# Performance work log

Hardware: AMD Instinct MI355X
Metric: run time of the kernel (lower is better)

The kernel has to match this reference:

```python
import jax, jax.numpy as jnp
import numpy as np
from jax import lax

B, CIN, COUT, FES, H, W, K = 32, 64, 64, 3, 128, 128, 3
DN = ('NCHW', 'OIHW', 'NCHW')
PAD = [(1, 1), (1, 1)]


def setup_inputs() -> dict:
    key = jax.random.key(0)
    ks = jax.random.split(key, 6)
    fan_main = CIN * K * K
    fan_extra = FES * K * K
    return {
        'x': jax.random.normal(ks[0], (B, CIN, H, W), jnp.float32),
        'extra_inputs': jax.random.normal(ks[1], (B, COUT * FES), jnp.float32),
        'conv_w': jax.random.normal(ks[2], (COUT, CIN, K, K), jnp.float32) / np.sqrt(fan_main),
        'conv_b': jax.random.normal(ks[3], (COUT,), jnp.float32) * 0.01,
        # extra_w[i] is the weight of extra_convs[i] (shape [1, FES, K, K]) stacked over i
        'extra_w': jax.random.normal(ks[4], (COUT, FES, K, K), jnp.float32) / np.sqrt(fan_extra),
        'extra_b': jax.random.normal(ks[5], (COUT,), jnp.float32) * 0.01,
    }


def reference(x, extra_inputs, conv_w, conv_b, extra_w, extra_b):
    # main conv: [B, CIN, H, W] -> [B, COUT, H, W]
    main_out = lax.conv_general_dilated(x, conv_w, (1, 1), PAD, dimension_numbers=DN)
    main_out = main_out + conv_b[None, :, None, None]

    b, _, h, w = x.shape
    cout = extra_w.shape[0]
    # spatially-constant broadcast of the per-sample embedding vector:
    # [B, COUT*FES] -> [B, COUT*FES, H, W]
    ein = jnp.broadcast_to(extra_inputs[:, :, None, None], (b, extra_inputs.shape[1], h, w))
    # the per-channel python loop of tiny convs == one grouped conv with
    # feature_group_count = COUT (each group: FES in-channels -> 1 out-channel)
    extra_out = lax.conv_general_dilated(ein, extra_w, (1, 1), PAD,
                                         dimension_numbers=DN,
                                         feature_group_count=cout)
    extra_out = extra_out + extra_b[None, :, None, None]
    return main_out + extra_out
```

## Files before the change

### kernel.cpp

```cpp
#include <hip/hip_runtime.h>

#define HH 128
#define WW 128
#define SB0 73728
#define SBN 26112

typedef __bf16 bf16x8 __attribute__((ext_vector_type(8)));
typedef __bf16 bf16x2 __attribute__((ext_vector_type(2)));
typedef float f32x4 __attribute__((ext_vector_type(4)));

static __device__ __forceinline__ unsigned short f2bf(float f) {
  unsigned int u = __float_as_uint(f);
  u = (u + 0x7FFFu + ((u >> 16) & 1u)) >> 16;
  return (unsigned short)u;
}

static __device__ __forceinline__ unsigned int pack2bf(float lo, float hi) {
  bf16x2 v;
  v[0] = (__bf16)lo;
  v[1] = (__bf16)hi;
  return __builtin_bit_cast(unsigned int, v);
}

__global__ __launch_bounds__(256) void prep_wfrag(const float* __restrict__ conv_w,
                                                  unsigned short* __restrict__ wfrag) {
  int tid = blockIdx.x * 256 + threadIdx.x;
  if (tid >= 18 * 2048) return;
  int i    = tid & 7;
  int lane = (tid >> 3) & 63;
  int cot  = (tid >> 9) & 3;
  int f    = tid >> 11;
  int h    = f / 9;
  int tap  = f - h * 9;
  int co   = cot * 16 + (lane & 15);
  int ci   = h * 32 + (lane >> 4) * 8 + i;
  wfrag[tid] = f2bf(conv_w[(co * 64 + ci) * 9 + tap]);
}

__global__ __launch_bounds__(256) void prep_ext(const float* __restrict__ extra_in,
                                                const float* __restrict__ extra_w,
                                                const float* __restrict__ conv_b,
                                                const float* __restrict__ extra_b,
                                                float* __restrict__ ext) {
  int t = blockIdx.x * 256 + threadIdx.x;
  if (t >= 32 * 64) return;
  int b = t >> 6, co = t & 63;
  float base = conv_b[co] + extra_b[co];
  float acc[3][3];
#pragma unroll
  for (int i = 0; i < 3; ++i)
#pragma unroll
    for (int j = 0; j < 3; ++j) acc[i][j] = 0.f;

#pragma unroll
  for (int f = 0; f < 3; ++f) {
    float e = extra_in[b * 192 + co * 3 + f];
    const float* w = extra_w + (co * 3 + f) * 9;
    float rs[3][3];
#pragma unroll
    for (int ky = 0; ky < 3; ++ky) {
      float w0 = w[ky * 3 + 0], w1 = w[ky * 3 + 1], w2 = w[ky * 3 + 2];
      rs[ky][0] = w1 + w2;
      rs[ky][1] = w0 + w1 + w2;
      rs[ky][2] = w0 + w1;
    }
#pragma unroll
    for (int cx = 0; cx < 3; ++cx) {
      acc[0][cx] += e * (rs[1][cx] + rs[2][cx]);
      acc[1][cx] += e * (rs[0][cx] + rs[1][cx] + rs[2][cx]);
      acc[2][cx] += e * (rs[0][cx] + rs[1][cx]);
    }
  }
#pragma unroll
  for (int cy = 0; cy < 3; ++cy)
#pragma unroll
    for (int cx = 0; cx < 3; ++cx)
      ext[t * 9 + cy * 3 + cx] = base + acc[cy][cx];
}

__global__ __launch_bounds__(512, 1) void conv_pc(const float* __restrict__ x,
                                                  const unsigned short* __restrict__ wfrag,
                                                  const float* __restrict__ ext,
                                                  float* __restrict__ out) {
  const int orig = blockIdx.x + 2 * (blockIdx.y + 4 * blockIdx.z);
  const int work = (orig & 7) * 32 + (orig >> 3);
  const int xh    = work & 1;
  const int yq    = (work >> 1) & 3;
  const int b     = work >> 3;

  const int ybase = yq * 32;
  const int x0    = xh * 64;
  const int tid  = threadIdx.x;
  const int lane = tid & 63;
  const int wv8  = tid >> 6;
  const int grp  = wv8 >> 2;
  const int wv   = wv8 & 3;
  const int gtid = tid & 255;
  const int pix  = lane & 15;
  const int g    = lane >> 4;

  __shared__ __align__(16) unsigned char lds[SB0 + 3 * SBN];

  const float* xb   = x + (size_t)b * 64 * HH * WW;
  const float* extb = ext + (size_t)b * 64 * 9;

#pragma unroll
  for (int it = 0; it < 9; ++it) {
    int off = (tid + it * 512) * 16;
    __builtin_amdgcn_global_load_lds(
        (const __attribute__((address_space(1))) unsigned int*)((const char*)wfrag + off),
        (__attribute__((address_space(3))) unsigned int*)(lds + off), 16, 0, 0);
  }

  auto stage_to = [&](int buf, int c, int h) {
    unsigned char* sb = lds + SB0 + buf * SBN;
#pragma unroll
    for (int it = 0; it < 2; ++it) {
      int q = gtid + it * 256;
      if (q < 384) {
        int qd  = q & 15;
        int cig = (q >> 4) & 3;
        int r   = q >> 6;
        int gy  = ybase + 4 * c - 1 + r;
        int cc  = 1 + 4 * qd;
        int x_in = x0 + 4 * qd;
        float4 f[8];
        if ((unsigned)gy < 128u) {
          const float* src = xb + (size_t)(h * 32 + cig * 8) * (HH * WW) + gy * WW + x_in;
#pragma unroll
          for (int j = 0; j < 8; ++j) f[j] = *(const float4*)(src + (size_t)j * (HH * WW));
        } else {
#pragma unroll
          for (int j = 0; j < 8; ++j) f[j] = make_float4(0.f, 0.f, 0.f, 0.f);
        }
#pragma unroll
        for (int p = 0; p < 4; ++p) {
          const int cp = cc + p;
          unsigned int pk[4];
#pragma unroll
          for (int w = 0; w < 4; ++w) {
            const float* lo = (const float*)&f[2 * w];
            const float* hi = (const float*)&f[2 * w + 1];
            pk[w] = pack2bf(lo[p], hi[p]);
          }
          int byte = ((r * 68 + cp) * 64 + cig * 16) ^ (((cp ^ (cp >> 2)) & 3) << 4);
          *(uint4*)(sb + byte) = make_uint4(pk[0], pk[1], pk[2], pk[3]);
        }
      }
    }
    if (gtid < 48) {
      int cc  = (gtid & 1) ? 65 : 0;
      int cig = (gtid >> 1) & 3;
      int r   = gtid >> 3;
      int gy  = ybase + 4 * c - 1 + r;
      int x_in = x0 - 1 + cc;
      bool inb = ((unsigned)gy < 128u) & ((unsigned)x_in < 128u);
      unsigned int pk[4] = {0u, 0u, 0u, 0u};
      if (inb) {
        const float* src = xb + (size_t)(h * 32 + cig * 8) * (HH * WW) + gy * WW + x_in;
        float v[8];
#pragma unroll
        for (int j = 0; j < 8; ++j) v[j] = src[(size_t)j * (HH * WW)];
#pragma unroll
        for (int w = 0; w < 4; ++w) pk[w] = pack2bf(v[2 * w], v[2 * w + 1]);
      }
      int byte = ((r * 68 + cc) * 64 + cig * 16) ^ (((cc ^ (cc >> 2)) & 3) << 4);
      *(uint4*)(sb + byte) = make_uint4(pk[0], pk[1], pk[2], pk[3]);
    }
  };

  if (grp == 0) stage_to(0, 0, 0);
  else          stage_to(1, 0, 1);
  __syncthreads();

  f32x4 acc[4][4];

#pragma unroll 1
  for (int p = 0; p < 16; ++p) {
    const int c = p >> 1, h = p & 1, buf = p % 3;
    if ((c & 1) == grp) {
      if (h == 0) {
#pragma unroll
        for (int i = 0; i < 4; ++i)
#pragma unroll
          for (int j = 0; j < 4; ++j) acc[i][j] = (f32x4){0.f, 0.f, 0.f, 0.f};
      }
      const unsigned char* sb = lds + SB0 + buf * SBN;
#pragma unroll
      for (int tap = 0; tap < 9; ++tap) {
        const int ky = tap / 3, kx = tap - ky * 3;
        bf16x8 af[4];
#pragma unroll
        for (int cot = 0; cot < 4; ++cot)
          af[cot] = *(const bf16x8*)(lds + (h * 9 + tap) * 4096 + cot * 1024 + lane * 16);
        bf16x8 pf[4];
        const int r = wv + ky;
#pragma unroll
        for (int m = 0; m < 4; ++m) {
          int cc = m * 16 + pix + kx;
          int byte = ((r * 68 + cc) * 64 + g * 16) ^ (((cc ^ (cc >> 2)) & 3) << 4);
          pf[m] = *(const bf16x8*)(sb + byte);
        }
#pragma unroll
        for (int cot = 0; cot < 4; ++cot)
#pragma unroll
          for (int m = 0; m < 4; ++m)
            acc[cot][m] = __builtin_amdgcn_mfma_f32_16x16x32_bf16(af[cot], pf[m],
                                                                  acc[cot][m], 0, 0, 0);
      }
      if (h == 1) {
        const int y  = ybase + 4 * c + wv;
        const int cy = (y == 0) ? 0 : ((y == HH - 1) ? 2 : 1);
#pragma unroll
        for (int cot = 0; cot < 4; ++cot) {
#pragma unroll
          for (int m = 0; m < 4; ++m) {
            int xg = x0 + m * 16 + pix;
            int cx = (xg == 0) ? 0 : ((xg == WW - 1) ? 2 : 1);
#pragma unroll
            for (int j = 0; j < 4; ++j) {
              int co = cot * 16 + g * 4 + j;
              out[(((size_t)b * 64 + co) * HH + y) * WW + xg] =
                  acc[cot][m][j] + extb[co * 9 + cy * 3 + cx];
            }
          }
        }
      }
    } else {
      const int p2 = p + 2;
      if (p2 < 16) stage_to(p2 % 3, p2 >> 1, p2 & 1);
    }
    __syncthreads();
  }
}

extern "C" void kernel_launch(void* const* d_in, const int* in_sizes, int n_in,
                              void* d_out, int out_size, void* d_ws, size_t ws_size,
                              hipStream_t stream) {
  const float* x        = (const float*)d_in[0];
  const float* extra_in = (const float*)d_in[1];
  const float* conv_w   = (const float*)d_in[2];
  const float* conv_b   = (const float*)d_in[3];
  const float* extra_w  = (const float*)d_in[4];
  const float* extra_b  = (const float*)d_in[5];
  float* out = (float*)d_out;

  unsigned short* wfrag = (unsigned short*)d_ws;
  float* ext = (float*)((char*)d_ws + 73728);

  hipLaunchKernelGGL(prep_wfrag, dim3(144), dim3(256), 0, stream, conv_w, wfrag);
  hipLaunchKernelGGL(prep_ext,   dim3(8),   dim3(256), 0, stream,
                     extra_in, extra_w, conv_b, extra_b, ext);
  hipLaunchKernelGGL(conv_pc, dim3(2, 4, 32), dim3(512), 0, stream,
                     x, wfrag, ext, out);
}
```

Baseline: 72.95 us.

## Split conv into many small blocks over output-channel halves and merge prep kernels

Replaces the persistent-style 256-block conv kernel (512 threads, triple-buffered LDS pipeline over 8 row chunks) with 4096 small 256-thread blocks. Each block handles 4 rows, 64 columns and one half of the output channels, with two blocks per CU. The aim is more blocks in flight and occupancy-based latency hiding in place of the explicit producer/consumer pipeline. In exchange, each input tile is loaded and bf16-converted twice (once per channel half), halo rows are re-read across row tiles, and weight fragments are reloaded per block. The two prep kernels are also fused into one launch.

Result: slower. 90.87 us (+24.6%).

```diff
diff --git a/kernel.cpp b/kernel.cpp
--- a/kernel.cpp
+++ b/kernel.cpp
@@ -2,8 +2,7 @@
 
 #define HH 128
 #define WW 128
-#define SB0 73728
-#define SBN 26112
+#define SBUF 36864
 
 typedef __bf16 bf16x8 __attribute__((ext_vector_type(8)));
 typedef __bf16 bf16x2 __attribute__((ext_vector_type(2)));
@@ -22,27 +21,28 @@
   return __builtin_bit_cast(unsigned int, v);
 }
 
-__global__ __launch_bounds__(256) void prep_wfrag(const float* __restrict__ conv_w,
-                                                  unsigned short* __restrict__ wfrag) {
-  int tid = blockIdx.x * 256 + threadIdx.x;
-  if (tid >= 18 * 2048) return;
-  int i    = tid & 7;
-  int lane = (tid >> 3) & 63;
-  int cot  = (tid >> 9) & 3;
-  int f    = tid >> 11;
-  int h    = f / 9;
-  int tap  = f - h * 9;
-  int co   = cot * 16 + (lane & 15);
-  int ci   = h * 32 + (lane >> 4) * 8 + i;
-  wfrag[tid] = f2bf(conv_w[(co * 64 + ci) * 9 + tap]);
-}
-
-__global__ __launch_bounds__(256) void prep_ext(const float* __restrict__ extra_in,
+__global__ __launch_bounds__(256) void prep_all(const float* __restrict__ conv_w,
+                                                const float* __restrict__ extra_in,
                                                 const float* __restrict__ extra_w,
                                                 const float* __restrict__ conv_b,
                                                 const float* __restrict__ extra_b,
+                                                unsigned short* __restrict__ wfrag,
                                                 float* __restrict__ ext) {
-  int t = blockIdx.x * 256 + threadIdx.x;
+  if (blockIdx.x < 144) {
+    int tid = blockIdx.x * 256 + threadIdx.x;
+    if (tid >= 18 * 2048) return;
+    int i    = tid & 7;
+    int lane = (tid >> 3) & 63;
+    int cot  = (tid >> 9) & 3;
+    int f    = tid >> 11;
+    int h    = f / 9;
+    int tap  = f - h * 9;
+    int co   = cot * 16 + (lane & 15);
+    int ci   = h * 32 + (lane >> 4) * 8 + i;
+    wfrag[tid] = f2bf(conv_w[(co * 64 + ci) * 9 + tap]);
+    return;
+  }
+  int t = (blockIdx.x - 144) * 256 + threadIdx.x;
   if (t >= 32 * 64) return;
   int b = t >> 6, co = t & 63;
   float base = conv_b[co] + extra_b[co];
@@ -51,7 +51,6 @@
   for (int i = 0; i < 3; ++i)
 #pragma unroll
     for (int j = 0; j < 3; ++j) acc[i][j] = 0.f;
-
 #pragma unroll
   for (int f = 0; f < 3; ++f) {
     float e = extra_in[b * 192 + co * 3 + f];
@@ -78,50 +77,49 @@
       ext[t * 9 + cy * 3 + cx] = base + acc[cy][cx];
 }
 
-__global__ __launch_bounds__(512, 1) void conv_pc(const float* __restrict__ x,
-                                                  const unsigned short* __restrict__ wfrag,
-                                                  const float* __restrict__ ext,
-                                                  float* __restrict__ out) {
-  const int orig = blockIdx.x + 2 * (blockIdx.y + 4 * blockIdx.z);
-  const int work = (orig & 7) * 32 + (orig >> 3);
-  const int xh    = work & 1;
-  const int yq    = (work >> 1) & 3;
-  const int b     = work >> 3;
-
-  const int ybase = yq * 32;
+__global__ __launch_bounds__(256, 2) void conv_half(const float* __restrict__ x,
+                                                    const unsigned short* __restrict__ wfrag,
+                                                    const float* __restrict__ ext,
+                                                    float* __restrict__ out) {
+  const int orig = blockIdx.x;
+  const int w    = (orig & 7) * 512 + (orig >> 3);
+  const int b    = w >> 7;
+  const int ch   = (w >> 6) & 1;
+  const int yt   = (w >> 1) & 31;
+  const int xh   = w & 1;
+
+  const int ybase = yt * 4;
   const int x0    = xh * 64;
   const int tid  = threadIdx.x;
   const int lane = tid & 63;
-  const int wv8  = tid >> 6;
-  const int grp  = wv8 >> 2;
-  const int wv   = wv8 & 3;
-  const int gtid = tid & 255;
+  const int wv   = tid >> 6;
   const int pix  = lane & 15;
   const int g    = lane >> 4;
 
-  __shared__ __align__(16) unsigned char lds[SB0 + 3 * SBN];
+  __shared__ __align__(16) unsigned char lds[SBUF + 26112];
 
   const float* xb   = x + (size_t)b * 64 * HH * WW;
   const float* extb = ext + (size_t)b * 64 * 9;
 
 #pragma unroll
   for (int it = 0; it < 9; ++it) {
-    int off = (tid + it * 512) * 16;
+    int d = (tid + it * 256) * 16;
+    int srcb = ((d >> 11) << 12) + (ch << 11) + (d & 2047);
     __builtin_amdgcn_global_load_lds(
-        (const __attribute__((address_space(1))) unsigned int*)((const char*)wfrag + off),
-        (__attribute__((address_space(3))) unsigned int*)(lds + off), 16, 0, 0);
-  }
-
-  auto stage_to = [&](int buf, int c, int h) {
-    unsigned char* sb = lds + SB0 + buf * SBN;
+        (const __attribute__((address_space(1))) unsigned int*)((const char*)wfrag + srcb),
+        (__attribute__((address_space(3))) unsigned int*)(lds + d), 16, 0, 0);
+  }
+
+  auto stage_half = [&](int h) {
+    unsigned char* sb = lds + SBUF;
 #pragma unroll
     for (int it = 0; it < 2; ++it) {
-      int q = gtid + it * 256;
+      int q = tid + it * 256;
       if (q < 384) {
         int qd  = q & 15;
         int cig = (q >> 4) & 3;
         int r   = q >> 6;
-        int gy  = ybase + 4 * c - 1 + r;
+        int gy  = ybase - 1 + r;
         int cc  = 1 + 4 * qd;
         int x_in = x0 + 4 * qd;
         float4 f[8];
@@ -138,21 +136,21 @@
           const int cp = cc + p;
           unsigned int pk[4];
 #pragma unroll
-          for (int w = 0; w < 4; ++w) {
-            const float* lo = (const float*)&f[2 * w];
-            const float* hi = (const float*)&f[2 * w + 1];
-            pk[w] = pack2bf(lo[p], hi[p]);
+          for (int ww = 0; ww < 4; ++ww) {
+            const float* lo = (const float*)&f[2 * ww];
+            const float* hi = (const float*)&f[2 * ww + 1];
+            pk[ww] = pack2bf(lo[p], hi[p]);
           }
           int byte = ((r * 68 + cp) * 64 + cig * 16) ^ (((cp ^ (cp >> 2)) & 3) << 4);
           *(uint4*)(sb + byte) = make_uint4(pk[0], pk[1], pk[2], pk[3]);
         }
       }
     }
-    if (gtid < 48) {
-      int cc  = (gtid & 1) ? 65 : 0;
-      int cig = (gtid >> 1) & 3;
-      int r   = gtid >> 3;
-      int gy  = ybase + 4 * c - 1 + r;
+    if (tid < 48) {
+      int cc  = (tid & 1) ? 65 : 0;
+      int cig = (tid >> 1) & 3;
+      int r   = tid >> 3;
+      int gy  = ybase - 1 + r;
       int x_in = x0 - 1 + cc;
       bool inb = ((unsigned)gy < 128u) & ((unsigned)x_in < 128u);
       unsigned int pk[4] = {0u, 0u, 0u, 0u};
@@ -162,75 +160,68 @@
 #pragma unroll
         for (int j = 0; j < 8; ++j) v[j] = src[(size_t)j * (HH * WW)];
 #pragma unroll
-        for (int w = 0; w < 4; ++w) pk[w] = pack2bf(v[2 * w], v[2 * w + 1]);
+        for (int ww = 0; ww < 4; ++ww) pk[ww] = pack2bf(v[2 * ww], v[2 * ww + 1]);
       }
       int byte = ((r * 68 + cc) * 64 + cig * 16) ^ (((cc ^ (cc >> 2)) & 3) << 4);
       *(uint4*)(sb + byte) = make_uint4(pk[0], pk[1], pk[2], pk[3]);
     }
   };
 
-  if (grp == 0) stage_to(0, 0, 0);
-  else          stage_to(1, 0, 1);
+  f32x4 acc[2][4];
+#pragma unroll
+  for (int i = 0; i < 2; ++i)
+#pragma unroll
+    for (int j = 0; j < 4; ++j) acc[i][j] = (f32x4){0.f, 0.f, 0.f, 0.f};
+
+  auto compute_half = [&](int h) {
+    const unsigned char* sb = lds + SBUF;
+#pragma unroll
+    for (int tap = 0; tap < 9; ++tap) {
+      const int ky = tap / 3, kx = tap - ky * 3;
+      bf16x8 af[2];
+#pragma unroll
+      for (int cotl = 0; cotl < 2; ++cotl)
+        af[cotl] = *(const bf16x8*)(lds + (h * 9 + tap) * 2048 + cotl * 1024 + lane * 16);
+      bf16x8 pf[4];
+      const int r = wv + ky;
+#pragma unroll
+      for (int m = 0; m < 4; ++m) {
+        int cc = m * 16 + pix + kx;
+        int byte = ((r * 68 + cc) * 64 + g * 16) ^ (((cc ^ (cc >> 2)) & 3) << 4);
+        pf[m] = *(const bf16x8*)(sb + byte);
+      }
+#pragma unroll
+      for (int cotl = 0; cotl < 2; ++cotl)
+#pragma unroll
+        for (int m = 0; m < 4; ++m)
+          acc[cotl][m] = __builtin_amdgcn_mfma_f32_16x16x32_bf16(af[cotl], pf[m],
+                                                                 acc[cotl][m], 0, 0, 0);
+    }
+  };
+
+  stage_half(0);
   __syncthreads();
-
-  f32x4 acc[4][4];
-
-#pragma unroll 1
-  for (int p = 0; p < 16; ++p) {
-    const int c = p >> 1, h = p & 1, buf = p % 3;
-    if ((c & 1) == grp) {
-      if (h == 0) {
-#pragma unroll
-        for (int i = 0; i < 4; ++i)
-#pragma unroll
-          for (int j = 0; j < 4; ++j) acc[i][j] = (f32x4){0.f, 0.f, 0.f, 0.f};
-      }
-      const unsigned char* sb = lds + SB0 + buf * SBN;
-#pragma unroll
-      for (int tap = 0; tap < 9; ++tap) {
-        const int ky = tap / 3, kx = tap - ky * 3;
-        bf16x8 af[4];
-#pragma unroll
-        for (int cot = 0; cot < 4; ++cot)
-          af[cot] = *(const bf16x8*)(lds + (h * 9 + tap) * 4096 + cot * 1024 + lane * 16);
-        bf16x8 pf[4];
-        const int r = wv + ky;
-#pragma unroll
-        for (int m = 0; m < 4; ++m) {
-          int cc = m * 16 + pix + kx;
-          int byte = ((r * 68 + cc) * 64 + g * 16) ^ (((cc ^ (cc >> 2)) & 3) << 4);
-          pf[m] = *(const bf16x8*)(sb + byte);
-        }
-#pragma unroll
-        for (int cot = 0; cot < 4; ++cot)
-#pragma unroll
-          for (int m = 0; m < 4; ++m)
-            acc[cot][m] = __builtin_amdgcn_mfma_f32_16x16x32_bf16(af[cot], pf[m],
-                                                                  acc[cot][m], 0, 0, 0);
-      }
-      if (h == 1) {
-        const int y  = ybase + 4 * c + wv;
-        const int cy = (y == 0) ? 0 : ((y == HH - 1) ? 2 : 1);
-#pragma unroll
-        for (int cot = 0; cot < 4; ++cot) {
-#pragma unroll
-          for (int m = 0; m < 4; ++m) {
-            int xg = x0 + m * 16 + pix;
-            int cx = (xg == 0) ? 0 : ((xg == WW - 1) ? 2 : 1);
-#pragma unroll
-            for (int j = 0; j < 4; ++j) {
-              int co = cot * 16 + g * 4 + j;
-              out[(((size_t)b * 64 + co) * HH + y) * WW + xg] =
-                  acc[cot][m][j] + extb[co * 9 + cy * 3 + cx];
-            }
-          }
-        }
-      }
-    } else {
-      const int p2 = p + 2;
-      if (p2 < 16) stage_to(p2 % 3, p2 >> 1, p2 & 1);
-    }
-    __syncthreads();
+  compute_half(0);
+  __syncthreads();
+  stage_half(1);
+  __syncthreads();
+  compute_half(1);
+
+  const int y  = ybase + wv;
+  const int cy = (y == 0) ? 0 : ((y == HH - 1) ? 2 : 1);
+#pragma unroll
+  for (int cotl = 0; cotl < 2; ++cotl) {
+#pragma unroll
+    for (int m = 0; m < 4; ++m) {
+      int xg = x0 + m * 16 + pix;
+      int cx = (xg == 0) ? 0 : ((xg == WW - 1) ? 2 : 1);
+#pragma unroll
+      for (int j = 0; j < 4; ++j) {
+        int co = ch * 32 + cotl * 16 + g * 4 + j;
+        out[(((size_t)b * 64 + co) * HH + y) * WW + xg] =
+            acc[cotl][m][j] + extb[co * 9 + cy * 3 + cx];
+      }
+    }
   }
 }
 
@@ -248,9 +239,8 @@
   unsigned short* wfrag = (unsigned short*)d_ws;
   float* ext = (float*)((char*)d_ws + 73728);
 
-  hipLaunchKernelGGL(prep_wfrag, dim3(144), dim3(256), 0, stream, conv_w, wfrag);
-  hipLaunchKernelGGL(prep_ext,   dim3(8),   dim3(256), 0, stream,
-                     extra_in, extra_w, conv_b, extra_b, ext);
-  hipLaunchKernelGGL(conv_pc, dim3(2, 4, 32), dim3(512), 0, stream,
+  hipLaunchKernelGGL(prep_all, dim3(152), dim3(256), 0, stream,
+                     conv_w, extra_in, extra_w, conv_b, extra_b, wfrag, ext);
+  hipLaunchKernelGGL(conv_half, dim3(4096), dim3(256), 0, stream,
                      x, wfrag, ext, out);
 }
```
